# Optimization experiments

Hardware: AMD Instinct MI355X
Metric: run time of the kernel (lower is better)

## Reference

```python
import jax, jax.numpy as jnp
import numpy as np

N = 262144          # total sentence instances
H = 256             # encoder hidden_dim
C = 128             # class_count
NUM_BAGS = 8192     # number of bags (segments)


def setup_inputs() -> dict:
    key = jax.random.key(0)
    k1, k2, k3, k4 = jax.random.split(key, 4)
    hidden = jax.random.normal(k1, (N, H), dtype=jnp.float32)
    W = jax.random.normal(k2, (C, H), dtype=jnp.float32) * 0.02
    b = jax.random.normal(k3, (C,), dtype=jnp.float32) * 0.02
    bag_id = jnp.sort(jax.random.randint(k4, (N,), 0, NUM_BAGS, dtype=jnp.int64))
    return {"hidden": hidden, "W": W, "b": b, "bag_id": bag_id}


def reference(hidden, W, b, bag_id):
    # Segment mean over bags (replaces the Python loop: hidden[bag_id == id].mean(0))
    sums = jax.ops.segment_sum(hidden, bag_id, num_segments=NUM_BAGS)          # [NUM_BAGS, H]
    counts = jax.ops.segment_sum(jnp.ones((hidden.shape[0],), hidden.dtype),
                                 bag_id, num_segments=NUM_BAGS)                # [NUM_BAGS]
    mean_hidden = sums / jnp.maximum(counts, 1.0)[:, None]                     # [NUM_BAGS, H]
    # classifier: nn.Linear(hidden_dim, class_count)
    select_logits = jnp.einsum('gh,ch->gc', mean_hidden, W) + b               # [NUM_BAGS, C]
    return select_logits
```

## Files before the change

kernel.cpp:

```cpp
#include <hip/hip_runtime.h>


#define NBAGS 8192
#define HDIM 256
#define CDIM 128
#define BPB 4

__global__ __launch_bounds__(256, 8) void bagre_kernel(
    const float* __restrict__ hidden,
    const float* __restrict__ W,
    const float* __restrict__ b,
    const int* __restrict__ bag_id,
    float* __restrict__ out,
    int N)
{
    __shared__ __align__(16) float s_mean[BPB][HDIM];
    __shared__ float s_part[2][BPB][CDIM];

    const int t    = threadIdx.x;
    const int g0   = blockIdx.x * BPB;
    const int wid  = t >> 6;
    const int lane = t & 63;

    int bound = 0;
    if (lane < 2) {
        const int target = g0 + wid + lane;
        int lo = 0, hi = N;
        while (lo < hi) {
            const int mid = (lo + hi) >> 1;
            if (bag_id[mid] < target) lo = mid + 1; else hi = mid;
        }
        bound = lo;
    }
    const int s = __shfl(bound, 0);
    const int e = __shfl(bound, 1);

    const int col4 = lane << 2;

    float4 a0 = make_float4(0.f, 0.f, 0.f, 0.f);
    float4 a1 = a0, a2 = a0, a3 = a0;

    const float* __restrict__ p = hidden + (size_t)s * HDIM + col4;
    int r = s;
    for (; r + 4 <= e; r += 4, p += 4 * HDIM) {
        const float4 v0 = *(const float4*)(p + 0 * HDIM);
        const float4 v1 = *(const float4*)(p + 1 * HDIM);
        const float4 v2 = *(const float4*)(p + 2 * HDIM);
        const float4 v3 = *(const float4*)(p + 3 * HDIM);
        a0.x += v0.x; a0.y += v0.y; a0.z += v0.z; a0.w += v0.w;
        a1.x += v1.x; a1.y += v1.y; a1.z += v1.z; a1.w += v1.w;
        a2.x += v2.x; a2.y += v2.y; a2.z += v2.z; a2.w += v2.w;
        a3.x += v3.x; a3.y += v3.y; a3.z += v3.z; a3.w += v3.w;
    }
    for (; r < e; ++r, p += HDIM) {
        const float4 v0 = *(const float4*)p;
        a0.x += v0.x; a0.y += v0.y; a0.z += v0.z; a0.w += v0.w;
    }

    const int cnt = e - s;
    const float inv = 1.0f / (float)(cnt > 1 ? cnt : 1);
    float4 m;
    m.x = (a0.x + a1.x + a2.x + a3.x) * inv;
    m.y = (a0.y + a1.y + a2.y + a3.y) * inv;
    m.z = (a0.z + a1.z + a2.z + a3.z) * inv;
    m.w = (a0.w + a1.w + a2.w + a3.w) * inv;
    *(float4*)(&s_mean[wid][col4]) = m;

    __syncthreads();

    const int c    = t & (CDIM - 1);
    const int half = t >> 7;
    const float* __restrict__ wrow = W + (size_t)c * HDIM + half * (HDIM / 2);

    float acc[BPB];
#pragma unroll
    for (int j = 0; j < BPB; ++j) acc[j] = 0.f;

    for (int hh = 0; hh < HDIM / 2; hh += 4) {
        const float4 wv = *(const float4*)(wrow + hh);
        const int hbase = half * (HDIM / 2) + hh;
#pragma unroll
        for (int j = 0; j < BPB; ++j) {
            acc[j] += s_mean[j][hbase + 0] * wv.x
                    + s_mean[j][hbase + 1] * wv.y
                    + s_mean[j][hbase + 2] * wv.z
                    + s_mean[j][hbase + 3] * wv.w;
        }
    }

#pragma unroll
    for (int j = 0; j < BPB; ++j) s_part[half][j][c] = acc[j];
    __syncthreads();

    for (int idx = t; idx < BPB * CDIM; idx += 256) {
        const int j  = idx >> 7;
        const int cc = idx & (CDIM - 1);
        out[(size_t)(g0 + j) * CDIM + cc] =
            s_part[0][j][cc] + s_part[1][j][cc] + b[cc];
    }
}

extern "C" void kernel_launch(void* const* d_in, const int* in_sizes, int n_in,
                              void* d_out, int out_size, void* d_ws, size_t ws_size,
                              hipStream_t stream) {
    const float* hidden = (const float*)d_in[0];
    const float* W      = (const float*)d_in[1];
    const float* b      = (const float*)d_in[2];
    const int*   bag_id = (const int*)d_in[3];
    float* out = (float*)d_out;
    const int N = in_sizes[3];

    bagre_kernel<<<NBAGS / BPB, 256, 0, stream>>>(hidden, W, b, bag_id, out, N);
}
```

Measured before the change: 391.3 us.

## Use persistent atomic-ticket blocks, wave-wide ballot search, and per-thread full-dot matvec

Replaces the one-block-per-chunk grid with 1024 persistent blocks that pull bag chunks through an atomic ticket counter, zeroed by a memset in workspace. The per-lane binary search is replaced by a three-level wave-wide ballot search over 64-way splits. The classifier stage now has each thread compute a full 256-long dot product for two bags, which removes the shared-memory partial reduction and one barrier. This adds a memset launch, a global atomic per chunk, and a hardcoded assumption that N is 262144 (64^3) in the search.

```diff
diff --git a/kernel.cpp b/kernel.cpp
--- a/kernel.cpp
+++ b/kernel.cpp
@@ -5,98 +5,100 @@
 #define HDIM 256
 #define CDIM 128
 #define BPB 4
+#define NCHUNK (NBAGS / BPB)
 
-__global__ __launch_bounds__(256, 8) void bagre_kernel(
+__device__ __forceinline__ int wide_lb(const int* __restrict__ bag_id,
+                                       int target, int lane)
+{
+    int v = bag_id[lane << 12];
+    int c = __popcll(__ballot(v < target));
+    int base = (c > 0 ? c - 1 : 0) << 12;
+
+    v = bag_id[base + (lane << 6)];
+    c = __popcll(__ballot(v < target));
+    base += (c > 0 ? c - 1 : 0) << 6;
+
+    v = bag_id[base + lane];
+    c = __popcll(__ballot(v < target));
+    return base + c;
+}
+
+__global__ __launch_bounds__(256) void bagre_kernel(
     const float* __restrict__ hidden,
     const float* __restrict__ W,
     const float* __restrict__ b,
     const int* __restrict__ bag_id,
     float* __restrict__ out,
+    int* __restrict__ ticket,
     int N)
 {
     __shared__ __align__(16) float s_mean[BPB][HDIM];
-    __shared__ float s_part[2][BPB][CDIM];
+    __shared__ int s_tk;
 
     const int t    = threadIdx.x;
-    const int g0   = blockIdx.x * BPB;
     const int wid  = t >> 6;
     const int lane = t & 63;
-
-    int bound = 0;
-    if (lane < 2) {
-        const int target = g0 + wid + lane;
-        int lo = 0, hi = N;
-        while (lo < hi) {
-            const int mid = (lo + hi) >> 1;
-            if (bag_id[mid] < target) lo = mid + 1; else hi = mid;
-        }
-        bound = lo;
-    }
-    const int s = __shfl(bound, 0);
-    const int e = __shfl(bound, 1);
-
     const int col4 = lane << 2;
 
-    float4 a0 = make_float4(0.f, 0.f, 0.f, 0.f);
-    float4 a1 = a0, a2 = a0, a3 = a0;
+    for (;;) {
+        if (t == 0) s_tk = atomicAdd(ticket, 1);
+        __syncthreads();
+        const int tk = s_tk;
+        if (tk >= NCHUNK) break;
+        const int g0 = tk * BPB;
 
-    const float* __restrict__ p = hidden + (size_t)s * HDIM + col4;
-    int r = s;
-    for (; r + 4 <= e; r += 4, p += 4 * HDIM) {
-        const float4 v0 = *(const float4*)(p + 0 * HDIM);
-        const float4 v1 = *(const float4*)(p + 1 * HDIM);
-        const float4 v2 = *(const float4*)(p + 2 * HDIM);
-        const float4 v3 = *(const float4*)(p + 3 * HDIM);
-        a0.x += v0.x; a0.y += v0.y; a0.z += v0.z; a0.w += v0.w;
-        a1.x += v1.x; a1.y += v1.y; a1.z += v1.z; a1.w += v1.w;
-        a2.x += v2.x; a2.y += v2.y; a2.z += v2.z; a2.w += v2.w;
-        a3.x += v3.x; a3.y += v3.y; a3.z += v3.z; a3.w += v3.w;
-    }
-    for (; r < e; ++r, p += HDIM) {
-        const float4 v0 = *(const float4*)p;
-        a0.x += v0.x; a0.y += v0.y; a0.z += v0.z; a0.w += v0.w;
-    }
+        const int g = g0 + wid;
+        const int s = wide_lb(bag_id, g, lane);
+        const int e = wide_lb(bag_id, g + 1, lane);
 
-    const int cnt = e - s;
-    const float inv = 1.0f / (float)(cnt > 1 ? cnt : 1);
-    float4 m;
-    m.x = (a0.x + a1.x + a2.x + a3.x) * inv;
-    m.y = (a0.y + a1.y + a2.y + a3.y) * inv;
-    m.z = (a0.z + a1.z + a2.z + a3.z) * inv;
-    m.w = (a0.w + a1.w + a2.w + a3.w) * inv;
-    *(float4*)(&s_mean[wid][col4]) = m;
+        float4 a0 = make_float4(0.f, 0.f, 0.f, 0.f);
+        float4 a1 = a0, a2 = a0, a3 = a0;
 
-    __syncthreads();
+        const float* __restrict__ p = hidden + (size_t)s * HDIM + col4;
+        int r = s;
+        for (; r + 4 <= e; r += 4, p += 4 * HDIM) {
+            const float4 v0 = *(const float4*)(p + 0 * HDIM);
+            const float4 v1 = *(const float4*)(p + 1 * HDIM);
+            const float4 v2 = *(const float4*)(p + 2 * HDIM);
+            const float4 v3 = *(const float4*)(p + 3 * HDIM);
+            a0.x += v0.x; a0.y += v0.y; a0.z += v0.z; a0.w += v0.w;
+            a1.x += v1.x; a1.y += v1.y; a1.z += v1.z; a1.w += v1.w;
+            a2.x += v2.x; a2.y += v2.y; a2.z += v2.z; a2.w += v2.w;
+            a3.x += v3.x; a3.y += v3.y; a3.z += v3.z; a3.w += v3.w;
+        }
+        for (; r < e; ++r, p += HDIM) {
+            const float4 v0 = *(const float4*)p;
+            a0.x += v0.x; a0.y += v0.y; a0.z += v0.z; a0.w += v0.w;
+        }
 
-    const int c    = t & (CDIM - 1);
-    const int half = t >> 7;
-    const float* __restrict__ wrow = W + (size_t)c * HDIM + half * (HDIM / 2);
+        const int cnt = e - s;
+        const float inv = 1.0f / (float)(cnt > 1 ? cnt : 1);
+        float4 m;
+        m.x = (a0.x + a1.x + a2.x + a3.x) * inv;
+        m.y = (a0.y + a1.y + a2.y + a3.y) * inv;
+        m.z = (a0.z + a1.z + a2.z + a3.z) * inv;
+        m.w = (a0.w + a1.w + a2.w + a3.w) * inv;
+        *(float4*)(&s_mean[wid][col4]) = m;
 
-    float acc[BPB];
-#pragma unroll
-    for (int j = 0; j < BPB; ++j) acc[j] = 0.f;
+        __syncthreads();
 
-    for (int hh = 0; hh < HDIM / 2; hh += 4) {
-        const float4 wv = *(const float4*)(wrow + hh);
-        const int hbase = half * (HDIM / 2) + hh;
-#pragma unroll
-        for (int j = 0; j < BPB; ++j) {
-            acc[j] += s_mean[j][hbase + 0] * wv.x
-                    + s_mean[j][hbase + 1] * wv.y
-                    + s_mean[j][hbase + 2] * wv.z
-                    + s_mean[j][hbase + 3] * wv.w;
+        {
+            const int c  = t & (CDIM - 1);
+            const int jb = (t >> 7) << 1;
+            const float* __restrict__ wrow = W + (size_t)c * HDIM;
+            float acc0 = 0.f, acc1 = 0.f;
+#pragma unroll 8
+            for (int k = 0; k < HDIM; k += 4) {
+                const float4 wv = *(const float4*)(wrow + k);
+                const float4 m0 = *(const float4*)(&s_mean[jb][k]);
+                const float4 m1 = *(const float4*)(&s_mean[jb + 1][k]);
+                acc0 += m0.x * wv.x + m0.y * wv.y + m0.z * wv.z + m0.w * wv.w;
+                acc1 += m1.x * wv.x + m1.y * wv.y + m1.z * wv.z + m1.w * wv.w;
+            }
+            const float bc = b[c];
+            out[(size_t)(g0 + jb)     * CDIM + c] = acc0 + bc;
+            out[(size_t)(g0 + jb + 1) * CDIM + c] = acc1 + bc;
         }
-    }
-
-#pragma unroll
-    for (int j = 0; j < BPB; ++j) s_part[half][j][c] = acc[j];
-    __syncthreads();
-
-    for (int idx = t; idx < BPB * CDIM; idx += 256) {
-        const int j  = idx >> 7;
-        const int cc = idx & (CDIM - 1);
-        out[(size_t)(g0 + j) * CDIM + cc] =
-            s_part[0][j][cc] + s_part[1][j][cc] + b[cc];
     }
 }
 
@@ -110,5 +112,7 @@
     float* out = (float*)d_out;
     const int N = in_sizes[3];
 
-    bagre_kernel<<<NBAGS / BPB, 256, 0, stream>>>(hidden, W, b, bag_id, out, N);
+    hipMemsetAsync(d_ws, 0, sizeof(int), stream);
+    bagre_kernel<<<1024, 256, 0, stream>>>(hidden, W, b, bag_id, out,
+                                           (int*)d_ws, N);
 }
```

New measurement: 429.7 us. 9.8% more time.
